# Kernel tuning notes

Hardware: AMD Instinct MI355X
Metric: run time of the kernel (lower is better)

## Reference

```python
import jax, jax.numpy as jnp
import numpy as np

B = 32       # batch_size
N = 8192     # points per set
D = 128      # d_in
LAM = 0.01   # lambda_ ridge regularizer


def setup_inputs() -> dict:
    key = jax.random.key(0)
    x = jax.random.normal(key, (B, N, D), dtype=jnp.float32)
    return {"x": x}


def reference(x):
    Bb, Nn, Dd = x.shape
    # mean-center over the point dim, then batched cov = diffs^T @ diffs / (N-1)
    diffs = x - x.mean(axis=1, keepdims=True)                  # (B, N, D)
    cov = jnp.einsum('bnd,bne->bde', diffs, diffs) / (Nn - 1)  # (B, D, D)
    cov = cov + LAM * jnp.eye(Dd, dtype=x.dtype)
    # torch.unique(dim=1) with generic float data: rows are all distinct,
    # so it reduces to a lexicographic ascending sort of the D rows.
    # jnp.lexsort uses the LAST key as primary -> reverse columns of m.T.
    idx = jax.vmap(lambda m: jnp.lexsort(m.T[::-1]))(cov)      # (B, D)
    sorted_cov = jnp.take_along_axis(cov, idx[:, :, None], axis=1)
    return sorted_cov.reshape(Bb, Dd * Dd)                     # (B, d_out)
```

## Files before the change

### kernel.cpp

```cpp
#include <hip/hip_runtime.h>
#include <hip/hip_bf16.h>

#define DD 128
#define NPTS 8192
#define BBATCH 32
#define BK 64
#define LAM 0.01f

typedef __attribute__((ext_vector_type(8))) short bf16x8;
typedef __attribute__((ext_vector_type(16))) float f32x16;

__device__ __forceinline__ unsigned f2bf_u(float f) {
    unsigned u = __builtin_bit_cast(unsigned, f);
    return (u + 0x7FFFu + ((u >> 16) & 1u)) >> 16;
}
__device__ __forceinline__ float bf2f(unsigned short u) {
    unsigned v = ((unsigned)u) << 16;
    return __builtin_bit_cast(float, v);
}
__device__ __forceinline__ int swz(int d) { return ((d >> 2) ^ d) & 7; }

#define ASM_BARRIER()  asm volatile("s_barrier" ::: "memory")
#define WAIT_VM4()     asm volatile("s_waitcnt vmcnt(4)" ::: "memory")
#define WAIT_VM0()     asm volatile("s_waitcnt vmcnt(0)" ::: "memory")
#define WAIT_LGKM0()   asm volatile("s_waitcnt lgkmcnt(0)" ::: "memory")

__device__ __forceinline__ void dma16(const void* g, void* l) {
    __builtin_amdgcn_global_load_lds(
        (const __attribute__((address_space(1))) void*)g,
        (__attribute__((address_space(3))) void*)l, 16, 0, 0);
}

template<int P>
__global__ __launch_bounds__(512) void gram_stats(
    const float* __restrict__ x, unsigned short* __restrict__ Spart,
    float* __restrict__ CSpart, float* __restrict__ KDpart)
{
    __shared__ char smem[3 * 32768 + 2 * 16384];
    short* XT = (short*)(smem + 98304);

    constexpr int rowsPerBlk = NPTS / P;
    constexpr int T = rowsPerBlk / BK;

    const int blk = blockIdx.x;
    const int b   = blk & 31;
    const int kc  = blk >> 5;
    const float* xb = x + (size_t)b * NPTS * DD + (size_t)(kc * rowsPerBlk) * DD;

    const int tid    = threadIdx.x;
    const int lane   = tid & 63;
    const int wave   = tid >> 6;
    const int dg     = tid & 31;
    const int rowgrp = tid >> 5;
    const int chunk  = rowgrp >> 1;
    const int wr32   = (wave & 3) * 32;
    const int wc64   = (wave >> 2) * 64;

    f32x16 acc0 = {}; f32x16 acc1 = {};
    float csum[4] = {0.f, 0.f, 0.f, 0.f};
    float kdot[4] = {0.f, 0.f, 0.f, 0.f};

    auto dmaTile = [&](int t) {
        const char* g = (const char*)(xb + (size_t)t * BK * DD) + wave * 4096 + lane * 16;
        char* l = smem + (t % 3) * 32768 + wave * 4096;
        dma16(g,        l);
        dma16(g + 1024, l + 1024);
        dma16(g + 2048, l + 2048);
        dma16(g + 3072, l + 3072);
    };

    dmaTile(0);
    dmaTile(1);

    for (int t = 0; t < T; ++t) {
        if (t < T - 1) { WAIT_VM4(); } else { WAIT_VM0(); }
        ASM_BARRIER();

        const float* rw = (const float*)(smem + (t % 3) * 32768);
        float4 R[4];
        float xk[4];
        #pragma unroll
        for (int r = 0; r < 4; ++r) {
            const int row = rowgrp * 4 + r;
            R[r]  = *(const float4*)(rw + row * DD + dg * 4);
            xk[r] = rw[row * DD];
        }
        short* Xb = XT + (t & 1) * 8192;
        #pragma unroll
        for (int i = 0; i < 4; ++i) {
            const float v0 = (&R[0].x)[i], v1 = (&R[1].x)[i];
            const float v2 = (&R[2].x)[i], v3 = (&R[3].x)[i];
            csum[i] += v0 + v1 + v2 + v3;
            kdot[i] += xk[0] * v0 + xk[1] * v1 + xk[2] * v2 + xk[3] * v3;
            const int d = 4 * dg + i;
            unsigned u0 = f2bf_u(v0) | (f2bf_u(v1) << 16);
            unsigned u1 = f2bf_u(v2) | (f2bf_u(v3) << 16);
            const int addr = d * BK + ((chunk ^ swz(d)) * 8) + (rowgrp & 1) * 4;
            uint2 vv; vv.x = u0; vv.y = u1;
            *(uint2*)(Xb + addr) = vv;
        }
        WAIT_LGKM0();
        ASM_BARRIER();

        if (t + 2 < T) dmaTile(t + 2);

        const short* Xc = XT + (t & 1) * 8192;
        #pragma unroll
        for (int ks = 0; ks < BK / 16; ++ks) {
            const int cb = ks * 2 + (lane >> 5);
            const int m = lane & 31;
            const int ad = wr32 + m, b0d = wc64 + m, b1d = wc64 + 32 + m;
            bf16x8 a  = *(const bf16x8*)(Xc + ad  * BK + ((cb ^ swz(ad))  * 8));
            bf16x8 b0 = *(const bf16x8*)(Xc + b0d * BK + ((cb ^ swz(b0d)) * 8));
            bf16x8 b1 = *(const bf16x8*)(Xc + b1d * BK + ((cb ^ swz(b1d)) * 8));
            acc0 = __builtin_amdgcn_mfma_f32_32x32x16_bf16(a, b0, acc0, 0, 0, 0);
            acc1 = __builtin_amdgcn_mfma_f32_32x32x16_bf16(a, b1, acc1, 0, 0, 0);
        }
    }

    unsigned short* Sp = Spart + ((size_t)b * P + kc) * (DD * DD);
    const int colLane = lane & 31;
    const int rowHw = 4 * (lane >> 5);
    #pragma unroll
    for (int r = 0; r < 16; ++r) {
        const int row = wr32 + (r & 3) + 8 * (r >> 2) + rowHw;
        Sp[row * DD + wc64 + colLane]      = (unsigned short)f2bf_u(acc0[r]);
        Sp[row * DD + wc64 + 32 + colLane] = (unsigned short)f2bf_u(acc1[r]);
    }

    __syncthreads();
    float* red = (float*)smem;
    #pragma unroll
    for (int i = 0; i < 4; ++i) {
        red[tid] = csum[i];
        __syncthreads();
        if (tid < 32) {
            float s = 0.f;
            #pragma unroll
            for (int g = 0; g < 16; ++g) s += red[g * 32 + tid];
            CSpart[((size_t)b * P + kc) * DD + 4 * tid + i] = s;
        }
        __syncthreads();
        red[tid] = kdot[i];
        __syncthreads();
        if (tid < 32) {
            float s = 0.f;
            #pragma unroll
            for (int g = 0; g < 16; ++g) s += red[g * 32 + tid];
            KDpart[((size_t)b * P + kc) * DD + 4 * tid + i] = s;
        }
        __syncthreads();
    }
}

template<int P>
__global__ __launch_bounds__(128) void keys_ranks(
    const float* __restrict__ CSpart, const float* __restrict__ KDpart,
    float* __restrict__ csOut, int* __restrict__ rankOut)
{
    __shared__ float csh[DD];
    __shared__ float key[DD];
    const int b = blockIdx.x;
    const int tid = threadIdx.x;
    float s = 0.f, kd = 0.f;
    #pragma unroll
    for (int p = 0; p < P; ++p) {
        s  += CSpart[((size_t)b * P + p) * DD + tid];
        kd += KDpart[((size_t)b * P + p) * DD + tid];
    }
    csh[tid] = s;
    __syncthreads();
    const float k = (kd - s * csh[0] * (1.f / NPTS)) * (1.f / (NPTS - 1))
                  + ((tid == 0) ? LAM : 0.f);
    key[tid] = k;
    __syncthreads();
    int r = 0;
    #pragma unroll 8
    for (int j = 0; j < DD; ++j) {
        const float kj = key[j];
        r += (kj < k) || (kj == k && j < tid);
    }
    csOut[b * DD + tid] = s;
    rankOut[b * DD + tid] = r;
}

template<int P>
__global__ __launch_bounds__(256) void reduce_scatter(
    const unsigned short* __restrict__ Spart, const float* __restrict__ csOut,
    const int* __restrict__ rankOut, float* __restrict__ out)
{
    __shared__ float csh[DD];
    __shared__ int rk[8];
    const int b = blockIdx.x;
    const int seg = blockIdx.y;
    const int tid = threadIdx.x;
    if (tid < DD) csh[tid] = csOut[b * DD + tid];
    if (tid < 8)  rk[tid] = rankOut[b * DD + seg * 8 + tid];

    const int base = seg * (8 * DD) + tid * 4;
    float a0 = 0.f, a1 = 0.f, a2 = 0.f, a3 = 0.f;
    #pragma unroll
    for (int p = 0; p < P; ++p) {
        uint2 v = *(const uint2*)(Spart + ((size_t)b * P + p) * (DD * DD) + base);
        a0 += bf2f((unsigned short)(v.x & 0xFFFFu));
        a1 += bf2f((unsigned short)(v.x >> 16));
        a2 += bf2f((unsigned short)(v.y & 0xFFFFu));
        a3 += bf2f((unsigned short)(v.y >> 16));
    }
    __syncthreads();
    const int row = seg * 8 + (tid >> 5);
    const int j0  = (tid & 31) * 4;
    const float ci = csh[row];
    const float invN = 1.f / NPTS, invNm1 = 1.f / (NPTS - 1);
    float4 v;
    v.x = (a0 - ci * csh[j0 + 0] * invN) * invNm1 + ((row == j0 + 0) ? LAM : 0.f);
    v.y = (a1 - ci * csh[j0 + 1] * invN) * invNm1 + ((row == j0 + 1) ? LAM : 0.f);
    v.z = (a2 - ci * csh[j0 + 2] * invN) * invNm1 + ((row == j0 + 2) ? LAM : 0.f);
    v.w = (a3 - ci * csh[j0 + 3] * invN) * invNm1 + ((row == j0 + 3) ? LAM : 0.f);
    float* o = out + (size_t)b * DD * DD + (size_t)rk[tid >> 5] * DD + j0;
    *(float4*)o = v;
}

template<int P>
static void launch_all(const float* x, float* out, void* d_ws, hipStream_t stream)
{
    size_t nS = (size_t)BBATCH * P * DD * DD;
    unsigned short* Spart = (unsigned short*)d_ws;
    float* CSpart = (float*)(Spart + nS);
    float* KDpart = CSpart + (size_t)BBATCH * P * DD;
    float* csOut  = KDpart + (size_t)BBATCH * P * DD;
    int*   rankOut = (int*)(csOut + (size_t)BBATCH * DD);

    gram_stats<P><<<dim3(32 * P), dim3(512), 0, stream>>>(x, Spart, CSpart, KDpart);
    keys_ranks<P><<<dim3(BBATCH), dim3(128), 0, stream>>>(CSpart, KDpart, csOut, rankOut);
    reduce_scatter<P><<<dim3(BBATCH, 16), dim3(256), 0, stream>>>(Spart, csOut, rankOut, out);
}

extern "C" void kernel_launch(void* const* d_in, const int* in_sizes, int n_in,
                              void* d_out, int out_size, void* d_ws, size_t ws_size,
                              hipStream_t stream)
{
    const float* x = (const float*)d_in[0];
    float* out = (float*)d_out;

    auto need = [](int P) {
        return (size_t)BBATCH * P * DD * DD * sizeof(unsigned short)
             + (size_t)BBATCH * P * 2 * DD * sizeof(float)
             + (size_t)BBATCH * DD * (sizeof(float) + sizeof(int));
    };
    if (need(8) <= ws_size)       launch_all<8>(x, out, d_ws, stream);
    else                          launch_all<4>(x, out, d_ws, stream);
}
```

Measured before the change: 202.3 us.

## Replace LDS DMA triple-buffering with register-prefetch pipeline and double the K-split

The gram kernel no longer copies fp32 tiles into a 96KB LDS ring with global_load_lds. Each thread now prefetches its tile slice straight into registers, two tiles ahead, and overlaps that with the MFMA phase on the other bf16 LDS buffer. The first-column value for the k-dot products now comes from a lane shuffle instead of an LDS read. With LDS use cut to 32KB, the kernel can set launch_bounds(512,4), and the point dimension is split into 16 partitions instead of 8 when the workspace allows. The aim is more blocks resident and better latency hiding of the memory-bound input stream. The cost is extra register pressure and twice as many partial Gram matrices for the reduce kernel.

```diff
diff --git a/kernel.cpp b/kernel.cpp
--- a/kernel.cpp
+++ b/kernel.cpp
@@ -21,24 +21,14 @@
 __device__ __forceinline__ int swz(int d) { return ((d >> 2) ^ d) & 7; }
 
 #define ASM_BARRIER()  asm volatile("s_barrier" ::: "memory")
-#define WAIT_VM4()     asm volatile("s_waitcnt vmcnt(4)" ::: "memory")
-#define WAIT_VM0()     asm volatile("s_waitcnt vmcnt(0)" ::: "memory")
 #define WAIT_LGKM0()   asm volatile("s_waitcnt lgkmcnt(0)" ::: "memory")
 
-__device__ __forceinline__ void dma16(const void* g, void* l) {
-    __builtin_amdgcn_global_load_lds(
-        (const __attribute__((address_space(1))) void*)g,
-        (__attribute__((address_space(3))) void*)l, 16, 0, 0);
-}
-
-template<int P>
-__global__ __launch_bounds__(512) void gram_stats(
+template<int P>
+__global__ __launch_bounds__(512, 4) void gram_stats(
     const float* __restrict__ x, unsigned short* __restrict__ Spart,
     float* __restrict__ CSpart, float* __restrict__ KDpart)
 {
-    __shared__ char smem[3 * 32768 + 2 * 16384];
-    short* XT = (short*)(smem + 98304);
-
+    __shared__ short XT[2][DD * BK];
     constexpr int rowsPerBlk = NPTS / P;
     constexpr int T = rowsPerBlk / BK;
 
@@ -59,39 +49,24 @@
     f32x16 acc0 = {}; f32x16 acc1 = {};
     float csum[4] = {0.f, 0.f, 0.f, 0.f};
     float kdot[4] = {0.f, 0.f, 0.f, 0.f};
-
-    auto dmaTile = [&](int t) {
-        const char* g = (const char*)(xb + (size_t)t * BK * DD) + wave * 4096 + lane * 16;
-        char* l = smem + (t % 3) * 32768 + wave * 4096;
-        dma16(g,        l);
-        dma16(g + 1024, l + 1024);
-        dma16(g + 2048, l + 2048);
-        dma16(g + 3072, l + 3072);
-    };
-
-    dmaTile(0);
-    dmaTile(1);
-
-    for (int t = 0; t < T; ++t) {
-        if (t < T - 1) { WAIT_VM4(); } else { WAIT_VM0(); }
-        ASM_BARRIER();
-
-        const float* rw = (const float*)(smem + (t % 3) * 32768);
-        float4 R[4];
-        float xk[4];
-        #pragma unroll
-        for (int r = 0; r < 4; ++r) {
-            const int row = rowgrp * 4 + r;
-            R[r]  = *(const float4*)(rw + row * DD + dg * 4);
-            xk[r] = rw[row * DD];
-        }
-        short* Xb = XT + (t & 1) * 8192;
+    float4 RA[4], RB[4];
+
+    auto issueLoads = [&](float4* R, int t) {
+        const float4* s = (const float4*)(xb + (size_t)(t * BK + rowgrp * 4) * DD) + dg;
+        R[0] = s[0]; R[1] = s[32]; R[2] = s[64]; R[3] = s[96];
+    };
+    auto convertStore = [&](float4* R, int buf) {
+        float x00 = __shfl(R[0].x, lane & 32);
+        float x01 = __shfl(R[1].x, lane & 32);
+        float x02 = __shfl(R[2].x, lane & 32);
+        float x03 = __shfl(R[3].x, lane & 32);
+        short* Xb = XT[buf];
         #pragma unroll
         for (int i = 0; i < 4; ++i) {
             const float v0 = (&R[0].x)[i], v1 = (&R[1].x)[i];
             const float v2 = (&R[2].x)[i], v3 = (&R[3].x)[i];
             csum[i] += v0 + v1 + v2 + v3;
-            kdot[i] += xk[0] * v0 + xk[1] * v1 + xk[2] * v2 + xk[3] * v3;
+            kdot[i] += x00 * v0 + x01 * v1 + x02 * v2 + x03 * v3;
             const int d = 4 * dg + i;
             unsigned u0 = f2bf_u(v0) | (f2bf_u(v1) << 16);
             unsigned u1 = f2bf_u(v2) | (f2bf_u(v3) << 16);
@@ -99,12 +74,8 @@
             uint2 vv; vv.x = u0; vv.y = u1;
             *(uint2*)(Xb + addr) = vv;
         }
-        WAIT_LGKM0();
-        ASM_BARRIER();
-
-        if (t + 2 < T) dmaTile(t + 2);
-
-        const short* Xc = XT + (t & 1) * 8192;
+    };
+    auto mfmaPhase = [&](const short* Xc) {
         #pragma unroll
         for (int ks = 0; ks < BK / 16; ++ks) {
             const int cb = ks * 2 + (lane >> 5);
@@ -116,6 +87,24 @@
             acc0 = __builtin_amdgcn_mfma_f32_32x32x16_bf16(a, b0, acc0, 0, 0, 0);
             acc1 = __builtin_amdgcn_mfma_f32_32x32x16_bf16(a, b1, acc1, 0, 0, 0);
         }
+    };
+
+    issueLoads(RA, 0);
+    issueLoads(RB, 1);
+    convertStore(RA, 0);
+    WAIT_LGKM0(); ASM_BARRIER();
+
+    for (int tt = 0; tt < T; tt += 2) {
+        if (tt + 2 < T) issueLoads(RA, tt + 2);
+        mfmaPhase(XT[0]);
+        convertStore(RB, 1);
+        WAIT_LGKM0(); ASM_BARRIER();
+        if (tt + 3 < T) issueLoads(RB, tt + 3);
+        mfmaPhase(XT[1]);
+        if (tt + 2 < T) {
+            convertStore(RA, 0);
+            WAIT_LGKM0(); ASM_BARRIER();
+        }
     }
 
     unsigned short* Sp = Spart + ((size_t)b * P + kc) * (DD * DD);
@@ -129,7 +118,7 @@
     }
 
     __syncthreads();
-    float* red = (float*)smem;
+    float* red = (float*)XT;
     #pragma unroll
     for (int i = 0; i < 4; ++i) {
         red[tid] = csum[i];
@@ -248,6 +237,6 @@
              + (size_t)BBATCH * P * 2 * DD * sizeof(float)
              + (size_t)BBATCH * DD * (sizeof(float) + sizeof(int));
     };
-    if (need(8) <= ws_size)       launch_all<8>(x, out, d_ws, stream);
-    else                          launch_all<4>(x, out, d_ws, stream);
-}
+    if (need(16) <= ws_size)      launch_all<16>(x, out, d_ws, stream);
+    else                          launch_all<8>(x, out, d_ws, stream);
+}
```

After: 200.5 us. About the same (-0.9%).
